# Kernel optimization log

Measured on AMD Instinct MI355X. Metric: run time of the kernel, lower is better.

## Reference

```python
import jax, jax.numpy as jnp
import numpy as np

RANK = 3
NUM_STEPS = 3
NUM_ENT = 40000
NUM_EMB = 24
NUM_OPS = 12
DIM = 128
HID = 128
BATCH = 128
NNZ = 300000


def _lstm_dir(x, Wih, Whh, bih, bhh, reverse=False):
    # x: (S, B, D); PyTorch gate order i, f, g, o
    B = x.shape[1]
    H = Whh.shape[1]
    def step(carry, xt):
        h, c = carry
        z = xt @ Wih.T + h @ Whh.T + bih + bhh  # (B, 4H)
        i, f, g, o = jnp.split(z, 4, axis=-1)
        c = jax.nn.sigmoid(f) * c + jax.nn.sigmoid(i) * jnp.tanh(g)
        h = jax.nn.sigmoid(o) * jnp.tanh(c)
        return (h, c), h
    init = (jnp.zeros((B, H), x.dtype), jnp.zeros((B, H), x.dtype))
    _, hs = jax.lax.scan(step, init, x, reverse=reverse)
    return hs  # (S, B, H)


def _spmm(memory, src, dst, val, num_ent):
    # memory: (B, E); edges (src -> dst): out[b, j] = sum_{e: dst[e]=j} memory[b, src[e]] * val[e]
    g = memory[:, src] * val[None, :]              # (B, nnz)
    out = jax.ops.segment_sum(g.T, dst, num_segments=num_ent)  # (E, B)
    return out.T


def setup_inputs() -> dict:
    key = jax.random.key(0)
    ks = jax.random.split(key, 16)
    inp = {
        'queries': jax.random.randint(ks[0], (BATCH,), 0, NUM_EMB),
        'heads': jax.random.randint(ks[1], (BATCH,), 0, NUM_ENT),
        'edge_src': jax.random.randint(ks[2], (NUM_OPS, NNZ), 0, NUM_ENT, dtype=jnp.int32),
        'edge_dst': jax.random.randint(ks[3], (NUM_OPS, NNZ), 0, NUM_ENT, dtype=jnp.int32),
        'edge_val': jax.random.uniform(ks[4], (NUM_OPS, NNZ), jnp.float32),
        'emb': jax.random.normal(ks[5], (NUM_EMB, DIM), jnp.float32) * 0.1,
        'Wih_f': jax.random.normal(ks[6], (RANK, 4 * HID, DIM), jnp.float32) * 0.1,
        'Whh_f': jax.random.normal(ks[7], (RANK, 4 * HID, HID), jnp.float32) * 0.1,
        'bih_f': jnp.zeros((RANK, 4 * HID), jnp.float32),
        'bhh_f': jnp.zeros((RANK, 4 * HID), jnp.float32),
        'Wih_b': jax.random.normal(ks[8], (RANK, 4 * HID, DIM), jnp.float32) * 0.1,
        'Whh_b': jax.random.normal(ks[9], (RANK, 4 * HID, HID), jnp.float32) * 0.1,
        'bih_b': jnp.zeros((RANK, 4 * HID), jnp.float32),
        'bhh_b': jnp.zeros((RANK, 4 * HID), jnp.float32),
        'W0': jax.random.normal(ks[10], (2 * HID, NUM_OPS + 1), jnp.float32) * 0.1,
        'b0': jnp.zeros((1, NUM_OPS + 1), jnp.float32),
    }
    return inp


def reference(queries, heads, edge_src, edge_dst, edge_val, emb,
              Wih_f, Whh_f, bih_f, bhh_f, Wih_b, Whh_b, bih_b, bhh_b, W0, b0):
    # query embedding replicated over time: (S, B, D)
    q = emb[queries]
    x = jnp.broadcast_to(q[None], (NUM_STEPS, q.shape[0], q.shape[1]))
    head_onehot = jax.nn.one_hot(heads, NUM_ENT, dtype=jnp.float32)  # (B, E)

    logits = jnp.zeros((q.shape[0], NUM_ENT), jnp.float32)
    for r in range(RANK):
        hf = _lstm_dir(x, Wih_f[r], Whh_f[r], bih_f[r], bhh_f[r], reverse=False)
        hb = _lstm_dir(x, Wih_b[r], Whh_b[r], bih_b[r], bhh_b[r], reverse=True)
        rnn_out = jnp.concatenate([hf, hb], axis=-1)          # (S, B, 2H)
        trans = rnn_out @ W0 + b0                             # (S, B, ops+1)
        attn = jax.nn.softmax(trans, axis=-1)
        attn = jnp.transpose(attn, (0, 2, 1))                 # (S, ops+1, B)

        memory = head_onehot                                  # (B, E)
        for t in range(NUM_STEPS):
            attn_t = attn[t]                                  # (ops+1, B)
            acc = memory * attn_t[-1][:, None]                # identity operator
            for op in range(NUM_OPS):
                prod = _spmm(memory, edge_src[op], edge_dst[op], edge_val[op], NUM_ENT)
                acc = acc + prod * attn_t[op][:, None]
            memory = acc
        norm = jnp.maximum(jnp.float32(1e-20), jnp.sum(memory, axis=1, keepdims=True))
        logits = logits + memory / norm
    return logits
```

## Files before the change

### kernel.cpp

```cpp
#include <hip/hip_runtime.h>

#define NENT 40000
#define NB 128
#define NQ 24
#define NOPS 12
#define EPO 300000
#define NTOT (NOPS * EPO)
#define NRANK 3
#define NPASS 8
#define CP 16
#define ECAP 160

typedef float v4f __attribute__((ext_vector_type(4)));

__device__ __forceinline__ v4f shfl_xor4(v4f x, int m) {
    v4f r;
    r.x = __shfl_xor(x.x, m);
    r.y = __shfl_xor(x.y, m);
    r.z = __shfl_xor(x.z, m);
    r.w = __shfl_xor(x.w, m);
    return r;
}

__device__ __forceinline__ bool bittest(const unsigned* bm, int i) {
    return (bm[i >> 5] >> (i & 31)) & 1u;
}

__global__ void headmark_kernel(const int* __restrict__ heads, unsigned* __restrict__ bmH,
                                unsigned* __restrict__ bm2) {
    int h = heads[threadIdx.x];
    atomicOr(&bmH[h >> 5], 1u << (h & 31));
    atomicOr(&bm2[h >> 5], 1u << (h & 31));
}

__global__ void mark2_kernel(const int* __restrict__ src, const int* __restrict__ dst,
                             const unsigned* __restrict__ bmH, unsigned* __restrict__ bm2) {
    int i = blockIdx.x * 256 + threadIdx.x;
    if (i < NTOT) {
        int s = src[i];
        if (bittest(bmH, s)) {
            int d = dst[i];
            atomicOr(&bm2[d >> 5], 1u << (d & 31));
        }
    }
}

__global__ void build_ell_kernel(const int* __restrict__ src, const int* __restrict__ dst,
                                 const float* __restrict__ val, const unsigned* __restrict__ bm2,
                                 int* __restrict__ fillD, int* __restrict__ fillS,
                                 int2* __restrict__ eD, int2* __restrict__ eS) {
    int i = blockIdx.x * 256 + threadIdx.x;
    if (i >= NTOT) return;
    int s = src[i], d = dst[i];
    int op = i / EPO;
    int v = __float_as_int(val[i]);
    int pd = atomicAdd(&fillD[d], 1);
    eD[(size_t)d * ECAP + pd] = make_int2(s | (op << 16), v);
    if (bittest(bm2, s)) {
        int ps = atomicAdd(&fillS[s], 1);
        eS[(size_t)s * ECAP + ps] = make_int2(d | (op << 16), v);
    }
}

__global__ void zxq_kernel(const float* __restrict__ emb,
                           const float* __restrict__ Wih_f, const float* __restrict__ bih_f,
                           const float* __restrict__ bhh_f,
                           const float* __restrict__ Wih_b, const float* __restrict__ bih_b,
                           const float* __restrict__ bhh_b,
                           float* __restrict__ zxq) {
    int combo = blockIdx.x / NQ;
    int q = blockIdx.x % NQ;
    int dir = combo / 3, r = combo % 3;
    const float* Wih = (dir ? Wih_b : Wih_f) + r * 512 * 128;
    const float* bih = (dir ? bih_b : bih_f) + r * 512;
    const float* bhh = (dir ? bhh_b : bhh_f) + r * 512;
    __shared__ float x[128];
    int u = threadIdx.x;
    x[u] = emb[q * 128 + u];
    __syncthreads();
    const float* W0p = Wih + u * 128;
    const float* W1p = Wih + (128 + u) * 128;
    const float* W2p = Wih + (256 + u) * 128;
    const float* W3p = Wih + (384 + u) * 128;
    float a0 = 0.f, a1 = 0.f, a2 = 0.f, a3 = 0.f;
    for (int d = 0; d < 128; ++d) {
        float xv = x[d];
        a0 = fmaf(xv, W0p[d], a0);
        a1 = fmaf(xv, W1p[d], a1);
        a2 = fmaf(xv, W2p[d], a2);
        a3 = fmaf(xv, W3p[d], a3);
    }
    float* o = zxq + (size_t)(combo * NQ + q) * 512;
    o[u]       = a0 + bih[u]       + bhh[u];
    o[128 + u] = a1 + bih[128 + u] + bhh[128 + u];
    o[256 + u] = a2 + bih[256 + u] + bhh[256 + u];
    o[384 + u] = a3 + bih[384 + u] + bhh[384 + u];
}

__global__ void lstmq_kernel(const float* __restrict__ Whh_f, const float* __restrict__ Whh_b,
                             const float* __restrict__ zxq, float* __restrict__ hq) {
    int combo = blockIdx.x / NQ;
    int q = blockIdx.x % NQ;
    int dir = combo / 3, r = combo % 3;
    const float* Whh = (dir ? Whh_b : Whh_f) + r * 512 * 128;
    __shared__ float h[128];
    int u = threadIdx.x;
    const float* z = zxq + (size_t)(combo * NQ + q) * 512;
    float zi0 = z[u], zf0 = z[128 + u], zg0 = z[256 + u], zo0 = z[384 + u];
    const float* Wi = Whh + u * 128;
    const float* Wf = Whh + (128 + u) * 128;
    const float* Wg = Whh + (256 + u) * 128;
    const float* Wo = Whh + (384 + u) * 128;
    float c = 0.f;
    h[u] = 0.f;
    for (int s = 0; s < 3; ++s) {
        __syncthreads();
        float a0 = 0.f, a1 = 0.f, a2 = 0.f, a3 = 0.f;
        for (int d = 0; d < 128; ++d) {
            float hv = h[d];
            a0 = fmaf(hv, Wi[d], a0);
            a1 = fmaf(hv, Wf[d], a1);
            a2 = fmaf(hv, Wg[d], a2);
            a3 = fmaf(hv, Wo[d], a3);
        }
        float ig = 1.f / (1.f + expf(-(zi0 + a0)));
        float fg = 1.f / (1.f + expf(-(zf0 + a1)));
        float gg = tanhf(zg0 + a2);
        float og = 1.f / (1.f + expf(-(zo0 + a3)));
        c = fg * c + ig * gg;
        float hn = og * tanhf(c);
        __syncthreads();
        h[u] = hn;
        hq[(size_t)((combo * 3 + s) * NQ + q) * 128 + u] = hn;
    }
}

__global__ void attnq_kernel(const float* __restrict__ hq, const float* __restrict__ W0,
                             const float* __restrict__ b0, float* __restrict__ attnq) {
    int r = blockIdx.x / 3, t = blockIdx.x % 3;
    __shared__ float W0s[256 * 13];
    for (int idx = threadIdx.x; idx < 256 * 13; idx += 32) W0s[idx] = W0[idx];
    __syncthreads();
    int q = threadIdx.x;
    if (q >= NQ) return;
    float acc[13];
    for (int k = 0; k < 13; ++k) acc[k] = b0[k];
    const float* hf = hq + (size_t)(((0 * 3 + r) * 3 + t) * NQ + q) * 128;
    const float* hb = hq + (size_t)(((1 * 3 + r) * 3 + (2 - t)) * NQ + q) * 128;
    for (int u = 0; u < 128; ++u) {
        float v = hf[u];
        for (int k = 0; k < 13; ++k) acc[k] = fmaf(v, W0s[u * 13 + k], acc[k]);
    }
    for (int u = 0; u < 128; ++u) {
        float v = hb[u];
        for (int k = 0; k < 13; ++k) acc[k] = fmaf(v, W0s[(128 + u) * 13 + k], acc[k]);
    }
    float m = acc[0];
    for (int k = 1; k < 13; ++k) m = fmaxf(m, acc[k]);
    float e[13];
    float sum = 0.f;
    for (int k = 0; k < 13; ++k) { e[k] = expf(acc[k] - m); sum += e[k]; }
    float inv = 1.f / sum;
    float* ao = attnq + (size_t)(r * 3 + t) * 13 * NQ;
    for (int k = 0; k < 13; ++k) ao[k * NQ + q] = e[k] * inv;
}

__global__ void expand_kernel(const int* __restrict__ queries, const float* __restrict__ attnq,
                              float* __restrict__ attn) {
    __shared__ int qs[128];
    if (threadIdx.x < 128) qs[threadIdx.x] = queries[threadIdx.x];
    __syncthreads();
    for (int idx = threadIdx.x; idx < 9 * 13 * 128; idx += 256) {
        int b = idx & 127, kk = idx >> 7;
        attn[idx] = attnq[kk * NQ + qs[b]];
    }
}

__global__ void fused01_kernel(const int* __restrict__ heads, const float* __restrict__ attn,
                               const int* __restrict__ fillS, const int2* __restrict__ eS,
                               float* __restrict__ mem2) {
    int r = blockIdx.y;
    int b = blockIdx.x;
    __shared__ float c0s[13], c1s[13];
    if (threadIdx.x < 13) {
        c0s[threadIdx.x] = attn[(size_t)((r * 3 + 0) * 13 + threadIdx.x) * 128 + b];
        c1s[threadIdx.x] = attn[(size_t)((r * 3 + 1) * 13 + threadIdx.x) * 128 + b];
    }
    __syncthreads();
    int h = heads[b];
    int lenH = fillS[h];
    float* mem = mem2 + ((size_t)(r * NPASS + (b >> 4)) * NENT) * CP + (b & 15);
    for (int ent = threadIdx.x; ent < lenH + 1; ent += 128) {
        int i; float wv;
        if (ent == 0) { i = h; wv = c0s[12]; }
        else {
            int2 e = eS[(size_t)h * ECAP + ent - 1];
            i = e.x & 0xFFFF;
            wv = __int_as_float(e.y) * c0s[e.x >> 16];
        }
        atomicAdd(&mem[(size_t)i * CP], c1s[12] * wv);
        int lenI = fillS[i];
        const int2* ei = eS + (size_t)i * ECAP;
        for (int f = 0; f < lenI; ++f) {
            int2 e2 = ei[f];
            atomicAdd(&mem[(size_t)(e2.x & 0xFFFF) * CP],
                      __int_as_float(e2.y) * c1s[e2.x >> 16] * wv);
        }
    }
}

__global__ __launch_bounds__(256) void dense_kernel(const float* __restrict__ attn,
                                                    const int* __restrict__ fillD,
                                                    const int2* __restrict__ edgesD,
                                                    const float* __restrict__ in,
                                                    float* __restrict__ out,
                                                    float* __restrict__ normv) {
    int p = blockIdx.x;
    int r = blockIdx.z;
    __shared__ __align__(16) float cs[13 * 20];
    __shared__ float npart[4][16];
    int tid = threadIdx.x;
    if (tid < 13 * 16) {
        int op = tid >> 4, c0 = tid & 15;
        cs[op * 20 + c0] = attn[(size_t)((r * 3 + 2) * 13 + op) * 128 + p * CP + c0];
    }
    __syncthreads();
    int wave = tid >> 6, lane = tid & 63;
    int slot = lane >> 2;
    int cq4 = (lane & 3) * 4;
    int jw = blockIdx.y * 32 + wave * 8;
    const float* inr = in + (size_t)(r * NPASS + p) * NENT * CP;
    float* outr = out + (size_t)(r * NPASS + p) * NENT * CP;
    int lens[8];
#pragma unroll
    for (int i = 0; i < 8; ++i) lens[i] = fillD[jw + i];
    v4f cid = *(const v4f*)&cs[12 * 20 + cq4];
    v4f rsum = (v4f)0.f;
#pragma unroll
    for (int rr = 0; rr < 8; ++rr) {
        int j = jw + rr;
        int len = lens[rr];
        const int2* ed = edgesD + (size_t)j * ECAP;
        v4f a = (v4f)0.f;
        for (int i = slot; i < len; i += 64) {
            int i1 = i + 16, i2 = i + 32, i3 = i + 48;
            bool m1 = i1 < len, m2 = i2 < len, m3 = i3 < len;
            int2 e0 = ed[i];
            int2 e1 = ed[m1 ? i1 : i];
            int2 e2 = ed[m2 ? i2 : i];
            int2 e3 = ed[m3 ? i3 : i];
            v4f g0 = *(const v4f*)(inr + (size_t)(e0.x & 0xFFFF) * CP + cq4);
            v4f g1 = *(const v4f*)(inr + (size_t)(e1.x & 0xFFFF) * CP + cq4);
            v4f g2 = *(const v4f*)(inr + (size_t)(e2.x & 0xFFFF) * CP + cq4);
            v4f g3 = *(const v4f*)(inr + (size_t)(e3.x & 0xFFFF) * CP + cq4);
            v4f c0 = *(const v4f*)&cs[(e0.x >> 16) * 20 + cq4];
            v4f c1 = *(const v4f*)&cs[(e1.x >> 16) * 20 + cq4];
            v4f c2 = *(const v4f*)&cs[(e2.x >> 16) * 20 + cq4];
            v4f c3 = *(const v4f*)&cs[(e3.x >> 16) * 20 + cq4];
            float v0 = __int_as_float(e0.y);
            float v1 = m1 ? __int_as_float(e1.y) : 0.f;
            float v2 = m2 ? __int_as_float(e2.y) : 0.f;
            float v3 = m3 ? __int_as_float(e3.y) : 0.f;
            a += (v0 * c0) * g0;
            a += (v1 * c1) * g1;
            a += (v2 * c2) * g2;
            a += (v3 * c3) * g3;
        }
        a += shfl_xor4(a, 4);
        a += shfl_xor4(a, 8);
        a += shfl_xor4(a, 16);
        a += shfl_xor4(a, 32);
        if (slot == 0) {
            v4f mi = *(const v4f*)(inr + (size_t)j * CP + cq4);
            v4f res = cid * mi + a;
            __builtin_nontemporal_store(res, (v4f*)(outr + (size_t)j * CP + cq4));
            rsum += res;
        }
    }
    if (slot == 0) *(v4f*)&npart[wave][cq4] = rsum;
    __syncthreads();
    if (tid < 16) {
        float s = npart[0][tid] + npart[1][tid] + npart[2][tid] + npart[3][tid];
        atomicAdd(&normv[r * 128 + p * CP + tid], s);
    }
}

__global__ void rnorm_kernel(const float* __restrict__ normv, float* __restrict__ rnormv) {
    int i = threadIdx.x;
    rnormv[i] = 1.f / fmaxf(normv[i], 1e-20f);
}

__global__ void final_kernel(const float* __restrict__ mem3, const float* __restrict__ rnormv,
                             float* __restrict__ out) {
    __shared__ float tile[32 * 129];
    __shared__ float rn[384];
    for (int idx = threadIdx.x; idx < 384; idx += 256) rn[idx] = rnormv[idx];
    __syncthreads();
    int j0 = blockIdx.x * 32;
    for (int p = 0; p < NPASS; ++p) {
        for (int it = 0; it < 2; ++it) {
            int lin = it * 256 + threadIdx.x;
            int jj = lin >> 4, c = lin & 15;
            int b = p * CP + c;
            float s = 0.f;
            for (int r = 0; r < 3; ++r)
                s += mem3[((size_t)(r * NPASS + p) * NENT + j0 + jj) * CP + c] * rn[r * 128 + b];
            tile[jj * 129 + b] = s;
        }
    }
    __syncthreads();
    for (int it = 0; it < 16; ++it) {
        int lin = it * 256 + threadIdx.x;
        int b = lin >> 5, jj = lin & 31;
        out[(size_t)b * NENT + j0 + jj] = tile[jj * 129 + b];
    }
}

extern "C" void kernel_launch(void* const* d_in, const int* in_sizes, int n_in,
                              void* d_out, int out_size, void* d_ws, size_t ws_size,
                              hipStream_t stream) {
    const int*   queries  = (const int*)d_in[0];
    const int*   heads    = (const int*)d_in[1];
    const int*   edge_src = (const int*)d_in[2];
    const int*   edge_dst = (const int*)d_in[3];
    const float* edge_val = (const float*)d_in[4];
    const float* emb      = (const float*)d_in[5];
    const float* Wih_f    = (const float*)d_in[6];
    const float* Whh_f    = (const float*)d_in[7];
    const float* bih_f    = (const float*)d_in[8];
    const float* bhh_f    = (const float*)d_in[9];
    const float* Wih_b    = (const float*)d_in[10];
    const float* Whh_b    = (const float*)d_in[11];
    const float* bih_b    = (const float*)d_in[12];
    const float* bhh_b    = (const float*)d_in[13];
    const float* W0       = (const float*)d_in[14];
    const float* b0       = (const float*)d_in[15];
    float* out = (float*)d_out;

    char* w = (char*)d_ws;
    size_t off = 0;
    auto alloc = [&](size_t bytes) -> void* {
        off = (off + 255) & ~(size_t)255;
        void* p = w + off;
        off += bytes;
        return p;
    };
    float* attnq  = (float*)alloc((size_t)9 * 13 * NQ * sizeof(float));
    float* attn   = (float*)alloc((size_t)9 * 13 * 128 * sizeof(float));
    float* zxq    = (float*)alloc((size_t)6 * NQ * 512 * sizeof(float));
    float* hq     = (float*)alloc((size_t)6 * 3 * NQ * 128 * sizeof(float));
    unsigned* bmH = (unsigned*)alloc((2 * 1250 + 2 * NENT) * sizeof(int));
    unsigned* bm2 = bmH + 1250;
    int* fillD    = (int*)(bm2 + 1250);
    int* fillS    = fillD + NENT;
    int2*  eD     = (int2*)alloc((size_t)NENT * ECAP * sizeof(int2));
    float* mem2   = (float*)alloc((size_t)NRANK * NENT * NB * sizeof(float));
    float* mem3   = (float*)alloc((size_t)NRANK * NENT * NB * sizeof(float));
    int2*  eS     = (int2*)mem3;
    float* normv  = (float*)alloc((size_t)NRANK * NB * sizeof(float));
    float* rnormv = (float*)alloc((size_t)NRANK * NB * sizeof(float));

    int cooGrid = (NTOT + 255) / 256;

    hipMemsetAsync(bmH, 0, (2 * 1250 + 2 * NENT) * sizeof(int), stream);
    headmark_kernel<<<1, 128, 0, stream>>>(heads, bmH, bm2);
    mark2_kernel<<<cooGrid, 256, 0, stream>>>(edge_src, edge_dst, bmH, bm2);
    build_ell_kernel<<<cooGrid, 256, 0, stream>>>(edge_src, edge_dst, edge_val, bm2,
                                                  fillD, fillS, eD, eS);

    zxq_kernel<<<6 * NQ, 128, 0, stream>>>(emb, Wih_f, bih_f, bhh_f, Wih_b, bih_b, bhh_b, zxq);
    lstmq_kernel<<<6 * NQ, 128, 0, stream>>>(Whh_f, Whh_b, zxq, hq);
    attnq_kernel<<<9, 32, 0, stream>>>(hq, W0, b0, attnq);
    expand_kernel<<<1, 256, 0, stream>>>(queries, attnq, attn);

    hipMemsetAsync(mem2, 0, (size_t)NRANK * NENT * NB * sizeof(float), stream);
    hipMemsetAsync(normv, 0, NRANK * NB * sizeof(float), stream);
    {
        dim3 g(NB, NRANK);
        fused01_kernel<<<g, 128, 0, stream>>>(heads, attn, fillS, eS, mem2);
    }
    {
        dim3 g(NPASS, NENT / 32, NRANK);
        dense_kernel<<<g, 256, 0, stream>>>(attn, fillD, eD, mem2, mem3, normv);
    }

    rnorm_kernel<<<1, NRANK * NB, 0, stream>>>(normv, rnormv);
    final_kernel<<<NENT / 32, 256, 0, stream>>>(mem3, rnormv, out);
}
```

Before: 1.283 ms.

## Segment fused01 into shared-memory accumulators, pad ELL rows, and merge small kernels

Rewrites the first two sparse propagation steps so each block accumulates one entity segment for all three ranks in LDS and writes the segment densely. This removes the memset of mem2 and the scattered global atomics, at the cost of every segment block re-walking the two-hop neighbourhood. It also pads dst-ELL rows to multiples of 16 so the dense loop drops per-edge bounds masks, with a scalar tail loop. Smaller changes fuse the LSTM input projection with the recurrence, fold the reciprocal norm into final_kernel, use nontemporal loads for COO reads, and switch the dense output store back to a normal store.

```diff
diff --git a/kernel.cpp b/kernel.cpp
--- a/kernel.cpp
+++ b/kernel.cpp
@@ -10,6 +10,7 @@
 #define NPASS 8
 #define CP 16
 #define ECAP 160
+#define SEG 5000
 
 typedef float v4f __attribute__((ext_vector_type(4)));
 
@@ -37,7 +38,7 @@
                              const unsigned* __restrict__ bmH, unsigned* __restrict__ bm2) {
     int i = blockIdx.x * 256 + threadIdx.x;
     if (i < NTOT) {
-        int s = src[i];
+        int s = __builtin_nontemporal_load(&src[i]);
         if (bittest(bmH, s)) {
             int d = dst[i];
             atomicOr(&bm2[d >> 5], 1u << (d & 31));
@@ -51,9 +52,10 @@
                                  int2* __restrict__ eD, int2* __restrict__ eS) {
     int i = blockIdx.x * 256 + threadIdx.x;
     if (i >= NTOT) return;
-    int s = src[i], d = dst[i];
+    int s = __builtin_nontemporal_load(&src[i]);
+    int d = __builtin_nontemporal_load(&dst[i]);
+    int v = __builtin_nontemporal_load((const int*)&val[i]);
     int op = i / EPO;
-    int v = __float_as_int(val[i]);
     int pd = atomicAdd(&fillD[d], 1);
     eD[(size_t)d * ECAP + pd] = make_int2(s | (op << 16), v);
     if (bittest(bm2, s)) {
@@ -62,51 +64,53 @@
     }
 }
 
-__global__ void zxq_kernel(const float* __restrict__ emb,
-                           const float* __restrict__ Wih_f, const float* __restrict__ bih_f,
-                           const float* __restrict__ bhh_f,
-                           const float* __restrict__ Wih_b, const float* __restrict__ bih_b,
-                           const float* __restrict__ bhh_b,
-                           float* __restrict__ zxq) {
+__global__ void pad_kernel(int* __restrict__ fillD, int2* __restrict__ eD) {
+    int j = blockIdx.x * 256 + threadIdx.x;
+    if (j >= NENT) return;
+    int l = fillD[j];
+    int lp = (l + 15) & ~15;
+    int2* row = eD + (size_t)j * ECAP;
+    for (int k = l; k < lp; ++k) row[k] = make_int2(0, 0);
+    fillD[j] = lp;
+}
+
+__global__ void lstm_all_kernel(const float* __restrict__ emb,
+                                const float* __restrict__ Wih_f, const float* __restrict__ bih_f,
+                                const float* __restrict__ bhh_f,
+                                const float* __restrict__ Wih_b, const float* __restrict__ bih_b,
+                                const float* __restrict__ bhh_b,
+                                const float* __restrict__ Whh_f, const float* __restrict__ Whh_b,
+                                float* __restrict__ hq) {
     int combo = blockIdx.x / NQ;
     int q = blockIdx.x % NQ;
     int dir = combo / 3, r = combo % 3;
     const float* Wih = (dir ? Wih_b : Wih_f) + r * 512 * 128;
     const float* bih = (dir ? bih_b : bih_f) + r * 512;
     const float* bhh = (dir ? bhh_b : bhh_f) + r * 512;
+    const float* Whh = (dir ? Whh_b : Whh_f) + r * 512 * 128;
     __shared__ float x[128];
+    __shared__ float h[128];
     int u = threadIdx.x;
     x[u] = emb[q * 128 + u];
     __syncthreads();
-    const float* W0p = Wih + u * 128;
-    const float* W1p = Wih + (128 + u) * 128;
-    const float* W2p = Wih + (256 + u) * 128;
-    const float* W3p = Wih + (384 + u) * 128;
     float a0 = 0.f, a1 = 0.f, a2 = 0.f, a3 = 0.f;
-    for (int d = 0; d < 128; ++d) {
-        float xv = x[d];
-        a0 = fmaf(xv, W0p[d], a0);
-        a1 = fmaf(xv, W1p[d], a1);
-        a2 = fmaf(xv, W2p[d], a2);
-        a3 = fmaf(xv, W3p[d], a3);
-    }
-    float* o = zxq + (size_t)(combo * NQ + q) * 512;
-    o[u]       = a0 + bih[u]       + bhh[u];
-    o[128 + u] = a1 + bih[128 + u] + bhh[128 + u];
-    o[256 + u] = a2 + bih[256 + u] + bhh[256 + u];
-    o[384 + u] = a3 + bih[384 + u] + bhh[384 + u];
-}
-
-__global__ void lstmq_kernel(const float* __restrict__ Whh_f, const float* __restrict__ Whh_b,
-                             const float* __restrict__ zxq, float* __restrict__ hq) {
-    int combo = blockIdx.x / NQ;
-    int q = blockIdx.x % NQ;
-    int dir = combo / 3, r = combo % 3;
-    const float* Whh = (dir ? Whh_b : Whh_f) + r * 512 * 128;
-    __shared__ float h[128];
-    int u = threadIdx.x;
-    const float* z = zxq + (size_t)(combo * NQ + q) * 512;
-    float zi0 = z[u], zf0 = z[128 + u], zg0 = z[256 + u], zo0 = z[384 + u];
+    {
+        const float* W0p = Wih + u * 128;
+        const float* W1p = Wih + (128 + u) * 128;
+        const float* W2p = Wih + (256 + u) * 128;
+        const float* W3p = Wih + (384 + u) * 128;
+        for (int d = 0; d < 128; ++d) {
+            float xv = x[d];
+            a0 = fmaf(xv, W0p[d], a0);
+            a1 = fmaf(xv, W1p[d], a1);
+            a2 = fmaf(xv, W2p[d], a2);
+            a3 = fmaf(xv, W3p[d], a3);
+        }
+    }
+    float zi0 = a0 + bih[u] + bhh[u];
+    float zf0 = a1 + bih[128 + u] + bhh[128 + u];
+    float zg0 = a2 + bih[256 + u] + bhh[256 + u];
+    float zo0 = a3 + bih[384 + u] + bhh[384 + u];
     const float* Wi = Whh + u * 128;
     const float* Wf = Whh + (128 + u) * 128;
     const float* Wg = Whh + (256 + u) * 128;
@@ -115,18 +119,18 @@
     h[u] = 0.f;
     for (int s = 0; s < 3; ++s) {
         __syncthreads();
-        float a0 = 0.f, a1 = 0.f, a2 = 0.f, a3 = 0.f;
+        float b0v = 0.f, b1v = 0.f, b2v = 0.f, b3v = 0.f;
         for (int d = 0; d < 128; ++d) {
             float hv = h[d];
-            a0 = fmaf(hv, Wi[d], a0);
-            a1 = fmaf(hv, Wf[d], a1);
-            a2 = fmaf(hv, Wg[d], a2);
-            a3 = fmaf(hv, Wo[d], a3);
-        }
-        float ig = 1.f / (1.f + expf(-(zi0 + a0)));
-        float fg = 1.f / (1.f + expf(-(zf0 + a1)));
-        float gg = tanhf(zg0 + a2);
-        float og = 1.f / (1.f + expf(-(zo0 + a3)));
+            b0v = fmaf(hv, Wi[d], b0v);
+            b1v = fmaf(hv, Wf[d], b1v);
+            b2v = fmaf(hv, Wg[d], b2v);
+            b3v = fmaf(hv, Wo[d], b3v);
+        }
+        float ig = 1.f / (1.f + expf(-(zi0 + b0v)));
+        float fg = 1.f / (1.f + expf(-(zf0 + b1v)));
+        float gg = tanhf(zg0 + b2v);
+        float og = 1.f / (1.f + expf(-(zo0 + b3v)));
         c = fg * c + ig * gg;
         float hn = og * tanhf(c);
         __syncthreads();
@@ -176,36 +180,65 @@
     }
 }
 
-__global__ void fused01_kernel(const int* __restrict__ heads, const float* __restrict__ attn,
-                               const int* __restrict__ fillS, const int2* __restrict__ eS,
-                               float* __restrict__ mem2) {
-    int r = blockIdx.y;
+__global__ __launch_bounds__(256) void fused01_kernel(const int* __restrict__ heads,
+                                                      const float* __restrict__ attn,
+                                                      const int* __restrict__ fillS,
+                                                      const int2* __restrict__ eS,
+                                                      float* __restrict__ mem2) {
+    __shared__ float acc3[3][SEG];
+    __shared__ float c0s[3][13], c1s[3][13];
     int b = blockIdx.x;
-    __shared__ float c0s[13], c1s[13];
-    if (threadIdx.x < 13) {
-        c0s[threadIdx.x] = attn[(size_t)((r * 3 + 0) * 13 + threadIdx.x) * 128 + b];
-        c1s[threadIdx.x] = attn[(size_t)((r * 3 + 1) * 13 + threadIdx.x) * 128 + b];
-    }
+    int seg = blockIdx.y;
+    int base = seg * SEG;
+    int tid = threadIdx.x;
+    if (tid < 39) {
+        int r = tid / 13, k = tid % 13;
+        c0s[r][k] = attn[(size_t)((r * 3 + 0) * 13 + k) * 128 + b];
+        c1s[r][k] = attn[(size_t)((r * 3 + 1) * 13 + k) * 128 + b];
+    }
+    for (int k = tid; k < 3 * SEG; k += 256) ((float*)acc3)[k] = 0.f;
     __syncthreads();
     int h = heads[b];
     int lenH = fillS[h];
-    float* mem = mem2 + ((size_t)(r * NPASS + (b >> 4)) * NENT) * CP + (b & 15);
-    for (int ent = threadIdx.x; ent < lenH + 1; ent += 128) {
-        int i; float wv;
-        if (ent == 0) { i = h; wv = c0s[12]; }
-        else {
+    for (int ent = tid; ent < lenH + 1; ent += 256) {
+        int i;
+        float wv0, wv1, wv2;
+        if (ent == 0) {
+            i = h;
+            wv0 = c0s[0][12]; wv1 = c0s[1][12]; wv2 = c0s[2][12];
+        } else {
             int2 e = eS[(size_t)h * ECAP + ent - 1];
             i = e.x & 0xFFFF;
-            wv = __int_as_float(e.y) * c0s[e.x >> 16];
-        }
-        atomicAdd(&mem[(size_t)i * CP], c1s[12] * wv);
+            float v = __int_as_float(e.y);
+            int op = e.x >> 16;
+            wv0 = v * c0s[0][op]; wv1 = v * c0s[1][op]; wv2 = v * c0s[2][op];
+        }
+        unsigned ti = (unsigned)(i - base);
+        if (ti < SEG) {
+            atomicAdd(&acc3[0][ti], c1s[0][12] * wv0);
+            atomicAdd(&acc3[1][ti], c1s[1][12] * wv1);
+            atomicAdd(&acc3[2][ti], c1s[2][12] * wv2);
+        }
         int lenI = fillS[i];
         const int2* ei = eS + (size_t)i * ECAP;
         for (int f = 0; f < lenI; ++f) {
             int2 e2 = ei[f];
-            atomicAdd(&mem[(size_t)(e2.x & 0xFFFF) * CP],
-                      __int_as_float(e2.y) * c1s[e2.x >> 16] * wv);
-        }
+            unsigned t = (unsigned)((e2.x & 0xFFFF) - base);
+            if (t < SEG) {
+                float v2 = __int_as_float(e2.y);
+                int op2 = e2.x >> 16;
+                atomicAdd(&acc3[0][t], v2 * c1s[0][op2] * wv0);
+                atomicAdd(&acc3[1][t], v2 * c1s[1][op2] * wv1);
+                atomicAdd(&acc3[2][t], v2 * c1s[2][op2] * wv2);
+            }
+        }
+    }
+    __syncthreads();
+    int p = b >> 4, c = b & 15;
+#pragma unroll
+    for (int r = 0; r < 3; ++r) {
+        float* dst = mem2 + ((size_t)(r * NPASS + p) * NENT + base) * CP + c;
+        for (int k = tid; k < SEG; k += 256) dst[(size_t)k * CP] = acc3[r][k];
     }
 }
 
@@ -242,13 +275,12 @@
         int len = lens[rr];
         const int2* ed = edgesD + (size_t)j * ECAP;
         v4f a = (v4f)0.f;
-        for (int i = slot; i < len; i += 64) {
-            int i1 = i + 16, i2 = i + 32, i3 = i + 48;
-            bool m1 = i1 < len, m2 = i2 < len, m3 = i3 < len;
+        int i = slot;
+        for (; i + 48 < len; i += 64) {
             int2 e0 = ed[i];
-            int2 e1 = ed[m1 ? i1 : i];
-            int2 e2 = ed[m2 ? i2 : i];
-            int2 e3 = ed[m3 ? i3 : i];
+            int2 e1 = ed[i + 16];
+            int2 e2 = ed[i + 32];
+            int2 e3 = ed[i + 48];
             v4f g0 = *(const v4f*)(inr + (size_t)(e0.x & 0xFFFF) * CP + cq4);
             v4f g1 = *(const v4f*)(inr + (size_t)(e1.x & 0xFFFF) * CP + cq4);
             v4f g2 = *(const v4f*)(inr + (size_t)(e2.x & 0xFFFF) * CP + cq4);
@@ -257,14 +289,16 @@
             v4f c1 = *(const v4f*)&cs[(e1.x >> 16) * 20 + cq4];
             v4f c2 = *(const v4f*)&cs[(e2.x >> 16) * 20 + cq4];
             v4f c3 = *(const v4f*)&cs[(e3.x >> 16) * 20 + cq4];
-            float v0 = __int_as_float(e0.y);
-            float v1 = m1 ? __int_as_float(e1.y) : 0.f;
-            float v2 = m2 ? __int_as_float(e2.y) : 0.f;
-            float v3 = m3 ? __int_as_float(e3.y) : 0.f;
-            a += (v0 * c0) * g0;
-            a += (v1 * c1) * g1;
-            a += (v2 * c2) * g2;
-            a += (v3 * c3) * g3;
+            a += (__int_as_float(e0.y) * c0) * g0;
+            a += (__int_as_float(e1.y) * c1) * g1;
+            a += (__int_as_float(e2.y) * c2) * g2;
+            a += (__int_as_float(e3.y) * c3) * g3;
+        }
+        for (; i < len; i += 16) {
+            int2 e0 = ed[i];
+            v4f g0 = *(const v4f*)(inr + (size_t)(e0.x & 0xFFFF) * CP + cq4);
+            v4f c0 = *(const v4f*)&cs[(e0.x >> 16) * 20 + cq4];
+            a += (__int_as_float(e0.y) * c0) * g0;
         }
         a += shfl_xor4(a, 4);
         a += shfl_xor4(a, 8);
@@ -273,7 +307,7 @@
         if (slot == 0) {
             v4f mi = *(const v4f*)(inr + (size_t)j * CP + cq4);
             v4f res = cid * mi + a;
-            __builtin_nontemporal_store(res, (v4f*)(outr + (size_t)j * CP + cq4));
+            *(v4f*)(outr + (size_t)j * CP + cq4) = res;
             rsum += res;
         }
     }
@@ -285,16 +319,12 @@
     }
 }
 
-__global__ void rnorm_kernel(const float* __restrict__ normv, float* __restrict__ rnormv) {
-    int i = threadIdx.x;
-    rnormv[i] = 1.f / fmaxf(normv[i], 1e-20f);
-}
-
-__global__ void final_kernel(const float* __restrict__ mem3, const float* __restrict__ rnormv,
+__global__ void final_kernel(const float* __restrict__ mem3, const float* __restrict__ normv,
                              float* __restrict__ out) {
     __shared__ float tile[32 * 129];
     __shared__ float rn[384];
-    for (int idx = threadIdx.x; idx < 384; idx += 256) rn[idx] = rnormv[idx];
+    for (int idx = threadIdx.x; idx < 384; idx += 256)
+        rn[idx] = 1.f / fmaxf(normv[idx], 1e-20f);
     __syncthreads();
     int j0 = blockIdx.x * 32;
     for (int p = 0; p < NPASS; ++p) {
@@ -347,7 +377,6 @@
     };
     float* attnq  = (float*)alloc((size_t)9 * 13 * NQ * sizeof(float));
     float* attn   = (float*)alloc((size_t)9 * 13 * 128 * sizeof(float));
-    float* zxq    = (float*)alloc((size_t)6 * NQ * 512 * sizeof(float));
     float* hq     = (float*)alloc((size_t)6 * 3 * NQ * 128 * sizeof(float));
     unsigned* bmH = (unsigned*)alloc((2 * 1250 + 2 * NENT) * sizeof(int));
     unsigned* bm2 = bmH + 1250;
@@ -358,7 +387,6 @@
     float* mem3   = (float*)alloc((size_t)NRANK * NENT * NB * sizeof(float));
     int2*  eS     = (int2*)mem3;
     float* normv  = (float*)alloc((size_t)NRANK * NB * sizeof(float));
-    float* rnormv = (float*)alloc((size_t)NRANK * NB * sizeof(float));
 
     int cooGrid = (NTOT + 255) / 256;
 
@@ -367,23 +395,22 @@
     mark2_kernel<<<cooGrid, 256, 0, stream>>>(edge_src, edge_dst, bmH, bm2);
     build_ell_kernel<<<cooGrid, 256, 0, stream>>>(edge_src, edge_dst, edge_val, bm2,
                                                   fillD, fillS, eD, eS);
-
-    zxq_kernel<<<6 * NQ, 128, 0, stream>>>(emb, Wih_f, bih_f, bhh_f, Wih_b, bih_b, bhh_b, zxq);
-    lstmq_kernel<<<6 * NQ, 128, 0, stream>>>(Whh_f, Whh_b, zxq, hq);
+    pad_kernel<<<(NENT + 255) / 256, 256, 0, stream>>>(fillD, eD);
+
+    lstm_all_kernel<<<6 * NQ, 128, 0, stream>>>(emb, Wih_f, bih_f, bhh_f,
+                                                Wih_b, bih_b, bhh_b, Whh_f, Whh_b, hq);
     attnq_kernel<<<9, 32, 0, stream>>>(hq, W0, b0, attnq);
     expand_kernel<<<1, 256, 0, stream>>>(queries, attnq, attn);
 
-    hipMemsetAsync(mem2, 0, (size_t)NRANK * NENT * NB * sizeof(float), stream);
     hipMemsetAsync(normv, 0, NRANK * NB * sizeof(float), stream);
     {
-        dim3 g(NB, NRANK);
-        fused01_kernel<<<g, 128, 0, stream>>>(heads, attn, fillS, eS, mem2);
+        dim3 g(NB, NENT / SEG);
+        fused01_kernel<<<g, 256, 0, stream>>>(heads, attn, fillS, eS, mem2);
     }
     {
         dim3 g(NPASS, NENT / 32, NRANK);
         dense_kernel<<<g, 256, 0, stream>>>(attn, fillD, eD, mem2, mem3, normv);
     }
 
-    rnorm_kernel<<<1, NRANK * NB, 0, stream>>>(normv, rnormv);
-    final_kernel<<<NENT / 32, 256, 0, stream>>>(mem3, rnormv, out);
-}
+    final_kernel<<<NENT / 32, 256, 0, stream>>>(mem3, normv, out);
+}
```

Measured after the change: 1.281 ms. Within noise of the previous version (-0.2%).
